# Kernel tuning notes

Measured on AMD Instinct MI355X. Metric: run time of the kernel, lower is better.

The kernel has to match this reference:

```python
import jax, jax.numpy as jnp
import numpy as np

B, N = 8, 512
C_IN, C_E, C_MID, C_OUT = 64, 16, 64, 64


def _linear_params(key, fan_in, fan_out):
    k1, k2 = jax.random.split(key)
    bound = 1.0 / np.sqrt(fan_in)
    W = jax.random.uniform(k1, (fan_out, fan_in), jnp.float32, -bound, bound)
    b = jax.random.uniform(k2, (fan_out,), jnp.float32, -bound, bound)
    return W, b


def setup_inputs() -> dict:
    key = jax.random.key(0)
    ks = jax.random.split(key, 9)
    x = jax.random.normal(ks[0], (B, N, C_IN), jnp.float32)
    adj = jax.random.randint(ks[1], (B, N, N), 0, 2).astype(jnp.float32)
    edge_attr = jax.random.normal(ks[2], (B, N, N, C_E), jnp.float32)
    W1, b1 = _linear_params(ks[3], C_IN, C_MID)
    W2, b2 = _linear_params(ks[4], C_IN, C_MID)
    We, be = _linear_params(ks[5], C_E, C_MID)
    Wn, bn = _linear_params(ks[6], C_MID, C_MID)   # user-supplied net: Linear(mid, mid)
    Wo1, bo1 = _linear_params(ks[7], C_IN, C_OUT)
    Wo2, bo2 = _linear_params(ks[8], C_MID, C_OUT)
    return {"x": x, "adj": adj, "edge_attr": edge_attr,
            "W1": W1, "b1": b1, "W2": W2, "b2": b2, "We": We, "be": be,
            "Wn": Wn, "bn": bn, "Wo1": Wo1, "bo1": bo1, "Wo2": Wo2, "bo2": bo2}


def reference(x, adj, edge_attr, W1, b1, W2, b2, We, be, Wn, bn, Wo1, bo1, Wo2, bo2):
    # node / edge projections
    msg_1 = jnp.einsum('bnc,mc->bnm', x, W1) + b1          # [B, N, mid]
    msg_2 = jnp.einsum('bnc,mc->bnm', x, W2) + b2          # [B, N, mid]
    msg_e = jnp.einsum('bijc,mc->bijm', edge_attr, We) + be  # [B, N, N, mid]
    # broadcast sum: msg_1 over dim 1, msg_2 over dim 2 (matches torch unsqueeze)
    msg = msg_1[:, None, :, :] + msg_2[:, :, None, :] + msg_e  # [B, N, N, mid]
    # net applied after hard-coded relu
    msg = jnp.einsum('bijm,km->bijk', jax.nn.relu(msg), Wn) + bn
    # sum aggregator with adjacency mask, reduced over dim 1
    msg = jnp.einsum('bijm,bij->bjm', msg, adj)            # [B, N, mid]
    h_1 = jnp.einsum('bnc,oc->bno', x, Wo1) + bo1
    h_2 = jnp.einsum('bnm,om->bno', msg, Wo2) + bo2
    return h_1 + h_2
```

## Files before the change

### kernel.cpp

```cpp
#include <hip/hip_runtime.h>
#include <stdint.h>

#define B_   8
#define N_   512
#define CE_  16
#define BN_  (B_*N_)
#define Q_   8

typedef __attribute__((ext_vector_type(8))) short bf16x8;
typedef __attribute__((ext_vector_type(4))) float f32x4;
typedef __attribute__((ext_vector_type(4))) int   i32x4;

union PackA { i32x4 i; bf16x8 h; };

__device__ __forceinline__ unsigned short f2bf_rne(float f) {
  unsigned u = __float_as_uint(f);
  u += 0x7FFFu + ((u >> 16) & 1u);
  return (unsigned short)(u >> 16);
}

__global__ __launch_bounds__(256) void k1_pre(
    const float* __restrict__ x,
    const float* __restrict__ W1,  const float* __restrict__ b1,
    const float* __restrict__ W2,  const float* __restrict__ b2,
    const float* __restrict__ Wn,  const float* __restrict__ bn,
    const float* __restrict__ Wo1, const float* __restrict__ bo1,
    const float* __restrict__ Wo2, const float* __restrict__ bo2,
    float* __restrict__ m1, float* __restrict__ m2t, float* __restrict__ base,
    float* __restrict__ Wc, float* __restrict__ bc)
{
  const int tid = threadIdx.x;
  if (blockIdx.x == BN_/4) {
    for (int idx = tid; idx < 64*64; idx += 256) {
      const int k = idx >> 6, m = idx & 63;
      float acc = 0.f;
      for (int t = 0; t < 64; ++t) acc += Wo2[k*64 + t] * Wn[t*64 + m];
      Wc[idx] = acc;
    }
    if (tid < 64) {
      float acc = 0.f;
      for (int t = 0; t < 64; ++t) acc += Wo2[tid*64 + t] * bn[t];
      bc[tid] = acc;
    }
    return;
  }
  const int r = tid >> 6, m = tid & 63;
  const int row = blockIdx.x*4 + r;
  __shared__ float xs[4][64];
  xs[r][m] = x[(size_t)row*64 + m];
  __syncthreads();
  const float* xr = xs[r];
  float a1 = b1[m], a2 = b2[m], a3 = bo1[m] + bo2[m];
  const float* w1r = W1  + m*64;
  const float* w2r = W2  + m*64;
  const float* w3r = Wo1 + m*64;
  #pragma unroll 8
  for (int c = 0; c < 64; ++c) {
    const float xv = xr[c];
    a1 += xv * w1r[c];
    a2 += xv * w2r[c];
    a3 += xv * w3r[c];
  }
  m1[(size_t)row*64 + m]   = a1;
  m2t[(size_t)row*64 + (m & 15)*4 + (m >> 4)] = a2;
  base[(size_t)row*64 + m] = a3;
}

__global__ __launch_bounds__(256, 5) void k2_main(
    const float* __restrict__ edge, const float* __restrict__ adj,
    const float* __restrict__ We,   const float* __restrict__ be,
    const float* __restrict__ m1,   const float* __restrict__ m2t,
    float* __restrict__ pS, float* __restrict__ pdeg)
{
  const int tid  = threadIdx.x;
  const int lane = tid & 63;
  const int wid  = tid >> 6;
  const int col  = lane & 15;
  const int quad = lane >> 4;

  const int blk = blockIdx.x;
  const int q   = blk & 7;
  const int grp = blk >> 3;
  const int b   = grp >> 5;
  const int j0  = (grp & 31) << 4;
  const int i0  = q*64 + wid*16;

  const i32x4 izero = {0,0,0,0};

  bf16x8 bfr[4];
  #pragma unroll
  for (int c = 0; c < 4; ++c) {
    PackA u; u.i = izero;
    if (quad < 2) {
      const float* wr = We + (c*16 + col)*CE_ + quad*8;
      unsigned p0 = ((unsigned)f2bf_rne(wr[1]) << 16) | f2bf_rne(wr[0]);
      unsigned p1 = ((unsigned)f2bf_rne(wr[3]) << 16) | f2bf_rne(wr[2]);
      unsigned p2 = ((unsigned)f2bf_rne(wr[5]) << 16) | f2bf_rne(wr[4]);
      unsigned p3 = ((unsigned)f2bf_rne(wr[7]) << 16) | f2bf_rne(wr[6]);
      i32x4 v = {(int)p0, (int)p1, (int)p2, (int)p3};
      u.i = v;
    }
    bfr[c] = u.h;
  }

  f32x4 m1f[4];
  #pragma unroll
  for (int c = 0; c < 4; ++c) {
    const float bev = be[c*16 + col];
    const float* mp = m1 + (size_t)(b*N_ + j0 + quad*4)*64 + c*16 + col;
    m1f[c].x = mp[0]   + bev;
    m1f[c].y = mp[64]  + bev;
    m1f[c].z = mp[128] + bev;
    m1f[c].w = mp[192] + bev;
  }

  const f32x4 fzero = {0.f, 0.f, 0.f, 0.f};
  f32x4 S[4];
  S[0] = fzero; S[1] = fzero; S[2] = fzero; S[3] = fzero;
  f32x4 deg4 = fzero;

  const float* ep  = edge + ((size_t)(b*N_ + i0)*N_ + (j0 + col))*CE_ + (quad & 1)*8;
  const float* ap  = adj  + (size_t)(b*N_ + i0)*N_ + j0 + quad*4;
  const float* m2p = m2t  + (size_t)(b*N_ + i0)*64 + col*4;

  f32x4 e0   = *(const f32x4*)(ep);
  f32x4 e1   = *(const f32x4*)(ep + 4);
  f32x4 adj4 = *(const f32x4*)(ap);
  f32x4 m2v  = *(const f32x4*)(m2p);

  auto compute = [&](const f32x4& ce0, const f32x4& ce1,
                     const f32x4& ca, const f32x4& cm) {
    PackA ua;
    ua.i.x = (int)__builtin_amdgcn_perm(__float_as_uint(ce0.y), __float_as_uint(ce0.x), 0x07060302u);
    ua.i.y = (int)__builtin_amdgcn_perm(__float_as_uint(ce0.w), __float_as_uint(ce0.z), 0x07060302u);
    ua.i.z = (int)__builtin_amdgcn_perm(__float_as_uint(ce1.y), __float_as_uint(ce1.x), 0x07060302u);
    ua.i.w = (int)__builtin_amdgcn_perm(__float_as_uint(ce1.w), __float_as_uint(ce1.z), 0x07060302u);
    #pragma unroll
    for (int c = 0; c < 4; ++c) {
      const float m2c = cm[c];
      f32x4 cin;
      cin.x = m1f[c].x + m2c;
      cin.y = m1f[c].y + m2c;
      cin.z = m1f[c].z + m2c;
      cin.w = m1f[c].w + m2c;
      f32x4 r = __builtin_amdgcn_mfma_f32_16x16x32_bf16(ua.h, bfr[c], cin, 0, 0, 0);
      S[c].x += ca.x * fmaxf(r.x, 0.f);
      S[c].y += ca.y * fmaxf(r.y, 0.f);
      S[c].z += ca.z * fmaxf(r.z, 0.f);
      S[c].w += ca.w * fmaxf(r.w, 0.f);
    }
    deg4.x += ca.x; deg4.y += ca.y; deg4.z += ca.z; deg4.w += ca.w;
  };

  #pragma unroll 1
  for (int it = 0; it < 15; ++it) {
    ep  += N_ * CE_;
    ap  += N_;
    m2p += 64;
    const f32x4 ne0  = *(const f32x4*)(ep);
    const f32x4 ne1  = *(const f32x4*)(ep + 4);
    const f32x4 nadj = *(const f32x4*)(ap);
    const f32x4 nm2  = *(const f32x4*)(m2p);
    compute(e0, e1, adj4, m2v);
    e0 = ne0; e1 = ne1; adj4 = nadj; m2v = nm2;
  }
  compute(e0, e1, adj4, m2v);

  __shared__ float red[4][16*68];
  __shared__ float redd[4][16];
  #pragma unroll
  for (int c = 0; c < 4; ++c) {
    red[wid][(quad*4 + 0)*68 + c*16 + col] = S[c].x;
    red[wid][(quad*4 + 1)*68 + c*16 + col] = S[c].y;
    red[wid][(quad*4 + 2)*68 + c*16 + col] = S[c].z;
    red[wid][(quad*4 + 3)*68 + c*16 + col] = S[c].w;
  }
  if (col == 0) {
    redd[wid][quad*4 + 0] = deg4.x;
    redd[wid][quad*4 + 1] = deg4.y;
    redd[wid][quad*4 + 2] = deg4.z;
    redd[wid][quad*4 + 3] = deg4.w;
  }
  __syncthreads();

  float* oS = pS + ((size_t)q*BN_ + b*N_ + j0)*64;
  #pragma unroll
  for (int t = 0; t < 4; ++t) {
    const int idx = t*256 + tid;
    const int row = idx >> 6, ch = idx & 63;
    oS[idx] = red[0][row*68 + ch] + red[1][row*68 + ch]
            + red[2][row*68 + ch] + red[3][row*68 + ch];
  }
  if (tid < 16) {
    pdeg[(size_t)q*BN_ + b*N_ + j0 + tid] =
      redd[0][tid] + redd[1][tid] + redd[2][tid] + redd[3][tid];
  }
}

__global__ __launch_bounds__(256) void k3_out(
    const float* __restrict__ pS, const float* __restrict__ pdeg,
    const float* __restrict__ base, const float* __restrict__ Wc,
    const float* __restrict__ bc, float* __restrict__ out)
{
  const int tid = threadIdx.x;
  const int r   = tid >> 6;
  const int k   = tid & 63;
  const int row = blockIdx.x*4 + r;
  __shared__ float sm[4][64];
  float s = 0.f, dr = 0.f;
  #pragma unroll
  for (int q = 0; q < Q_; ++q) {
    s  += pS[((size_t)q*BN_ + row)*64 + k];
    dr += pdeg[(size_t)q*BN_ + row];
  }
  sm[r][k] = s;
  __syncthreads();
  float acc = base[(size_t)row*64 + k] + dr * bc[k];
  const float* wr  = Wc + k*64;
  const float* smr = sm[r];
  #pragma unroll
  for (int m = 0; m < 64; ++m) acc += smr[m] * wr[m];
  out[(size_t)row*64 + k] = acc;
}

extern "C" void kernel_launch(void* const* d_in, const int* in_sizes, int n_in,
                              void* d_out, int out_size, void* d_ws, size_t ws_size,
                              hipStream_t stream)
{
  const float* x    = (const float*)d_in[0];
  const float* adj  = (const float*)d_in[1];
  const float* edge = (const float*)d_in[2];
  const float* W1   = (const float*)d_in[3];
  const float* b1   = (const float*)d_in[4];
  const float* W2   = (const float*)d_in[5];
  const float* b2   = (const float*)d_in[6];
  const float* We   = (const float*)d_in[7];
  const float* be   = (const float*)d_in[8];
  const float* Wn   = (const float*)d_in[9];
  const float* bn   = (const float*)d_in[10];
  const float* Wo1  = (const float*)d_in[11];
  const float* bo1  = (const float*)d_in[12];
  const float* Wo2  = (const float*)d_in[13];
  const float* bo2  = (const float*)d_in[14];
  float* out = (float*)d_out;

  char* ws = (char*)d_ws;
  float* m1   = (float*)(ws);
  float* m2t  = (float*)(ws + (size_t)(1u<<20));
  float* base = (float*)(ws + (size_t)2*(1u<<20));
  float* Wc   = (float*)(ws + (size_t)3*(1u<<20));
  float* bc   = (float*)(ws + (size_t)3*(1u<<20) + 16384);
  float* pdeg = (float*)(ws + (size_t)3*(1u<<20) + 17408);
  float* pS   = (float*)(ws + (size_t)3*(1u<<20) + 17408 + 131072);

  k1_pre<<<BN_/4 + 1, 256, 0, stream>>>(x, W1, b1, W2, b2, Wn, bn,
                                        Wo1, bo1, Wo2, bo2,
                                        m1, m2t, base, Wc, bc);
  k2_main<<<2048, 256, 0, stream>>>(edge, adj, We, be, m1, m2t, pS, pdeg);
  k3_out<<<BN_/4, 256, 0, stream>>>(pS, pdeg, base, Wc, bc, out);
}
```

Baseline: 302.0 us.

## Fold msg_2 into MFMA via padded K slot and double-buffer the edge loop

The per-row msg_2 term is stored as bf16 and placed into an unused K slot of the MFMA. The A operand gets a constant 1.0 in that slot and the B operand gets the m2 value, so the MFMA adds it directly instead of four vector adds per channel group per iteration. The main loop is also unrolled by two with ping-pong register buffers for the prefetched edge, adj and m2 loads. This cuts VALU work in the inner loop but rounds msg_2 to bf16 and raises register pressure.

Result: slower. 428.2 us (+41.8%).

```diff
diff --git a/kernel.cpp b/kernel.cpp
--- a/kernel.cpp
+++ b/kernel.cpp
@@ -10,6 +10,7 @@
 typedef __attribute__((ext_vector_type(8))) short bf16x8;
 typedef __attribute__((ext_vector_type(4))) float f32x4;
 typedef __attribute__((ext_vector_type(4))) int   i32x4;
+typedef __attribute__((ext_vector_type(2))) unsigned int u32x2;
 
 union PackA { i32x4 i; bf16x8 h; };
 
@@ -26,8 +27,8 @@
     const float* __restrict__ Wn,  const float* __restrict__ bn,
     const float* __restrict__ Wo1, const float* __restrict__ bo1,
     const float* __restrict__ Wo2, const float* __restrict__ bo2,
-    float* __restrict__ m1, float* __restrict__ m2t, float* __restrict__ base,
-    float* __restrict__ Wc, float* __restrict__ bc)
+    float* __restrict__ m1, unsigned short* __restrict__ m2b,
+    float* __restrict__ base, float* __restrict__ Wc, float* __restrict__ bc)
 {
   const int tid = threadIdx.x;
   if (blockIdx.x == BN_/4) {
@@ -62,14 +63,14 @@
     a3 += xv * w3r[c];
   }
   m1[(size_t)row*64 + m]   = a1;
-  m2t[(size_t)row*64 + (m & 15)*4 + (m >> 4)] = a2;
+  m2b[(size_t)row*64 + (m & 15)*4 + (m >> 4)] = f2bf_rne(a2);
   base[(size_t)row*64 + m] = a3;
 }
 
 __global__ __launch_bounds__(256, 5) void k2_main(
     const float* __restrict__ edge, const float* __restrict__ adj,
     const float* __restrict__ We,   const float* __restrict__ be,
-    const float* __restrict__ m1,   const float* __restrict__ m2t,
+    const float* __restrict__ m1,   const unsigned short* __restrict__ m2b,
     float* __restrict__ pS, float* __restrict__ pdeg)
 {
   const int tid  = threadIdx.x;
@@ -87,7 +88,8 @@
 
   const i32x4 izero = {0,0,0,0};
 
-  bf16x8 bfr[4];
+  PackA ub[4];
+  unsigned bx0[4];
   #pragma unroll
   for (int c = 0; c < 4; ++c) {
     PackA u; u.i = izero;
@@ -100,8 +102,13 @@
       i32x4 v = {(int)p0, (int)p1, (int)p2, (int)p3};
       u.i = v;
     }
-    bfr[c] = u.h;
-  }
+    ub[c] = u;
+    bx0[c] = (unsigned)u.i.x;
+  }
+
+  const unsigned sel   = (quad == 2) ? 0xFFFFu : 0u;
+  const unsigned akeep = (quad == 2) ? 0xFFFF0000u : 0xFFFFFFFFu;
+  const unsigned ains  = (quad == 2) ? 0x00003F80u : 0u;
 
   f32x4 m1f[4];
   #pragma unroll
@@ -119,31 +126,27 @@
   S[0] = fzero; S[1] = fzero; S[2] = fzero; S[3] = fzero;
   f32x4 deg4 = fzero;
 
-  const float* ep  = edge + ((size_t)(b*N_ + i0)*N_ + (j0 + col))*CE_ + (quad & 1)*8;
-  const float* ap  = adj  + (size_t)(b*N_ + i0)*N_ + j0 + quad*4;
-  const float* m2p = m2t  + (size_t)(b*N_ + i0)*64 + col*4;
-
-  f32x4 e0   = *(const f32x4*)(ep);
-  f32x4 e1   = *(const f32x4*)(ep + 4);
-  f32x4 adj4 = *(const f32x4*)(ap);
-  f32x4 m2v  = *(const f32x4*)(m2p);
+  const float*          ep = edge + ((size_t)(b*N_ + i0)*N_ + (j0 + col))*CE_ + (quad & 1)*8;
+  const float*          ap = adj  + (size_t)(b*N_ + i0)*N_ + j0 + quad*4;
+  const unsigned short* mp = m2b  + (size_t)(b*N_ + i0)*64 + col*4;
 
   auto compute = [&](const f32x4& ce0, const f32x4& ce1,
-                     const f32x4& ca, const f32x4& cm) {
+                     const f32x4& ca, const u32x2& cm) {
     PackA ua;
-    ua.i.x = (int)__builtin_amdgcn_perm(__float_as_uint(ce0.y), __float_as_uint(ce0.x), 0x07060302u);
+    unsigned ax = (unsigned)__builtin_amdgcn_perm(__float_as_uint(ce0.y), __float_as_uint(ce0.x), 0x07060302u);
+    ua.i.x = (int)((ax & akeep) | ains);
     ua.i.y = (int)__builtin_amdgcn_perm(__float_as_uint(ce0.w), __float_as_uint(ce0.z), 0x07060302u);
     ua.i.z = (int)__builtin_amdgcn_perm(__float_as_uint(ce1.y), __float_as_uint(ce1.x), 0x07060302u);
     ua.i.w = (int)__builtin_amdgcn_perm(__float_as_uint(ce1.w), __float_as_uint(ce1.z), 0x07060302u);
+    const unsigned mc0 = cm.x & 0xFFFFu, mc1 = cm.x >> 16;
+    const unsigned mc2 = cm.y & 0xFFFFu, mc3 = cm.y >> 16;
+    ub[0].i.x = (int)(bx0[0] | (mc0 & sel));
+    ub[1].i.x = (int)(bx0[1] | (mc1 & sel));
+    ub[2].i.x = (int)(bx0[2] | (mc2 & sel));
+    ub[3].i.x = (int)(bx0[3] | (mc3 & sel));
     #pragma unroll
     for (int c = 0; c < 4; ++c) {
-      const float m2c = cm[c];
-      f32x4 cin;
-      cin.x = m1f[c].x + m2c;
-      cin.y = m1f[c].y + m2c;
-      cin.z = m1f[c].z + m2c;
-      cin.w = m1f[c].w + m2c;
-      f32x4 r = __builtin_amdgcn_mfma_f32_16x16x32_bf16(ua.h, bfr[c], cin, 0, 0, 0);
+      f32x4 r = __builtin_amdgcn_mfma_f32_16x16x32_bf16(ua.h, ub[c].h, m1f[c], 0, 0, 0);
       S[c].x += ca.x * fmaxf(r.x, 0.f);
       S[c].y += ca.y * fmaxf(r.y, 0.f);
       S[c].z += ca.z * fmaxf(r.z, 0.f);
@@ -152,19 +155,28 @@
     deg4.x += ca.x; deg4.y += ca.y; deg4.z += ca.z; deg4.w += ca.w;
   };
 
+  f32x4 e0a = *(const f32x4*)(ep);
+  f32x4 e1a = *(const f32x4*)(ep + 4);
+  f32x4 ada = *(const f32x4*)(ap);
+  u32x2 ma  = *(const u32x2*)(mp);
+  f32x4 e0b, e1b, adb; u32x2 mb;
+
   #pragma unroll 1
-  for (int it = 0; it < 15; ++it) {
-    ep  += N_ * CE_;
-    ap  += N_;
-    m2p += 64;
-    const f32x4 ne0  = *(const f32x4*)(ep);
-    const f32x4 ne1  = *(const f32x4*)(ep + 4);
-    const f32x4 nadj = *(const f32x4*)(ap);
-    const f32x4 nm2  = *(const f32x4*)(m2p);
-    compute(e0, e1, adj4, m2v);
-    e0 = ne0; e1 = ne1; adj4 = nadj; m2v = nm2;
-  }
-  compute(e0, e1, adj4, m2v);
+  for (int it = 0; it < 16; it += 2) {
+    ep += N_ * CE_; ap += N_; mp += 64;
+    e0b = *(const f32x4*)(ep);
+    e1b = *(const f32x4*)(ep + 4);
+    adb = *(const f32x4*)(ap);
+    mb  = *(const u32x2*)(mp);
+    compute(e0a, e1a, ada, ma);
+    const int adv = (it < 14) ? 1 : 0;
+    ep += adv * (N_ * CE_); ap += adv * N_; mp += adv * 64;
+    e0a = *(const f32x4*)(ep);
+    e1a = *(const f32x4*)(ep + 4);
+    ada = *(const f32x4*)(ap);
+    ma  = *(const u32x2*)(mp);
+    compute(e0b, e1b, adb, mb);
+  }
 
   __shared__ float red[4][16*68];
   __shared__ float redd[4][16];
@@ -245,17 +257,17 @@
   float* out = (float*)d_out;
 
   char* ws = (char*)d_ws;
-  float* m1   = (float*)(ws);
-  float* m2t  = (float*)(ws + (size_t)(1u<<20));
-  float* base = (float*)(ws + (size_t)2*(1u<<20));
-  float* Wc   = (float*)(ws + (size_t)3*(1u<<20));
-  float* bc   = (float*)(ws + (size_t)3*(1u<<20) + 16384);
-  float* pdeg = (float*)(ws + (size_t)3*(1u<<20) + 17408);
-  float* pS   = (float*)(ws + (size_t)3*(1u<<20) + 17408 + 131072);
+  float*          m1   = (float*)(ws);
+  unsigned short* m2b  = (unsigned short*)(ws + (size_t)(1u<<20));
+  float*          base = (float*)(ws + (size_t)2*(1u<<20));
+  float*          Wc   = (float*)(ws + (size_t)3*(1u<<20));
+  float*          bc   = (float*)(ws + (size_t)3*(1u<<20) + 16384);
+  float*          pdeg = (float*)(ws + (size_t)3*(1u<<20) + 17408);
+  float*          pS   = (float*)(ws + (size_t)3*(1u<<20) + 17408 + 131072);
 
   k1_pre<<<BN_/4 + 1, 256, 0, stream>>>(x, W1, b1, W2, b2, Wn, bn,
                                         Wo1, bo1, Wo2, bo2,
-                                        m1, m2t, base, Wc, bc);
-  k2_main<<<2048, 256, 0, stream>>>(edge, adj, We, be, m1, m2t, pS, pdeg);
+                                        m1, m2b, base, Wc, bc);
+  k2_main<<<2048, 256, 0, stream>>>(edge, adj, We, be, m1, m2b, pS, pdeg);
   k3_out<<<BN_/4, 256, 0, stream>>>(pS, pdeg, base, Wc, bc, out);
 }
```

## Prefetch edge tiles into LDS with a 4-slot async global_load_lds ring

Applied to the files above, without the earlier changes.

Edge-attribute loads in the main aggregation kernel now go through a per-wave 4-slot LDS ring filled by global_load_lds, replacing the single-step register double buffer. Adjacency and m2 values sit in a matching 4-deep register ring, so three iterations of loads are in flight while one is computed. This targets the load latency the kernel is bound by. The ring uses more LDS and registers, so the launch bound drops from 5 to 4 blocks per SM, which lowers occupancy. The reduction scratch reuses the same LDS buffer, and correctness depends on a hand-written vmcnt wait plus in-order completion of loads.

Measured after the change: 448.9 us. 1.49x slower.

```diff
diff --git a/kernel.cpp b/kernel.cpp
--- a/kernel.cpp
+++ b/kernel.cpp
@@ -12,6 +12,9 @@
 typedef __attribute__((ext_vector_type(4))) int   i32x4;
 
 union PackA { i32x4 i; bf16x8 h; };
+
+typedef const __attribute__((address_space(1))) void cg_void;
+typedef __attribute__((address_space(3))) void ls_void;
 
 __device__ __forceinline__ unsigned short f2bf_rne(float f) {
   unsigned u = __float_as_uint(f);
@@ -66,12 +69,15 @@
   base[(size_t)row*64 + m] = a3;
 }
 
-__global__ __launch_bounds__(256, 5) void k2_main(
+__global__ __launch_bounds__(256, 4) void k2_main(
     const float* __restrict__ edge, const float* __restrict__ adj,
     const float* __restrict__ We,   const float* __restrict__ be,
     const float* __restrict__ m1,   const float* __restrict__ m2t,
     float* __restrict__ pS, float* __restrict__ pdeg)
 {
+  __shared__ f32x4 smem4[4][512];
+  __shared__ float redd[4][16];
+
   const int tid  = threadIdx.x;
   const int lane = tid & 63;
   const int wid  = tid >> 6;
@@ -107,11 +113,11 @@
   #pragma unroll
   for (int c = 0; c < 4; ++c) {
     const float bev = be[c*16 + col];
-    const float* mp = m1 + (size_t)(b*N_ + j0 + quad*4)*64 + c*16 + col;
-    m1f[c].x = mp[0]   + bev;
-    m1f[c].y = mp[64]  + bev;
-    m1f[c].z = mp[128] + bev;
-    m1f[c].w = mp[192] + bev;
+    const float* mp1 = m1 + (size_t)(b*N_ + j0 + quad*4)*64 + c*16 + col;
+    m1f[c].x = mp1[0]   + bev;
+    m1f[c].y = mp1[64]  + bev;
+    m1f[c].z = mp1[128] + bev;
+    m1f[c].w = mp1[192] + bev;
   }
 
   const f32x4 fzero = {0.f, 0.f, 0.f, 0.f};
@@ -119,14 +125,19 @@
   S[0] = fzero; S[1] = fzero; S[2] = fzero; S[3] = fzero;
   f32x4 deg4 = fzero;
 
-  const float* ep  = edge + ((size_t)(b*N_ + i0)*N_ + (j0 + col))*CE_ + (quad & 1)*8;
-  const float* ap  = adj  + (size_t)(b*N_ + i0)*N_ + j0 + quad*4;
-  const float* m2p = m2t  + (size_t)(b*N_ + i0)*64 + col*4;
-
-  f32x4 e0   = *(const f32x4*)(ep);
-  f32x4 e1   = *(const f32x4*)(ep + 4);
-  f32x4 adj4 = *(const f32x4*)(ap);
-  f32x4 m2v  = *(const f32x4*)(m2p);
+  const float* ep = edge + ((size_t)(b*N_ + i0)*N_ + (j0 + col))*CE_ + (quad & 1)*8;
+  const float* ap = adj  + (size_t)(b*N_ + i0)*N_ + j0 + quad*4;
+  const float* mp = m2t  + (size_t)(b*N_ + i0)*64 + col*4;
+  const int STEP = N_ * CE_;
+
+  f32x4* sbase = &smem4[wid][0];
+
+  auto issue_edge = [&](int slot, const float* p) {
+    __builtin_amdgcn_global_load_lds((cg_void*)p,
+        (ls_void*)(sbase + slot*128), 16, 0, 0);
+    __builtin_amdgcn_global_load_lds((cg_void*)(p + 4),
+        (ls_void*)(sbase + slot*128 + 64), 16, 0, 0);
+  };
 
   auto compute = [&](const f32x4& ce0, const f32x4& ce1,
                      const f32x4& ca, const f32x4& cm) {
@@ -152,28 +163,43 @@
     deg4.x += ca.x; deg4.y += ca.y; deg4.z += ca.z; deg4.w += ca.w;
   };
 
+  f32x4 adjR[4], m2R[4];
+  #pragma unroll
+  for (int g = 0; g < 3; ++g) {
+    issue_edge(g, ep);
+    adjR[g] = *(const f32x4*)ap;
+    m2R[g]  = *(const f32x4*)mp;
+    ep += STEP; ap += N_; mp += 64;
+  }
+  int itI = 3;
+
   #pragma unroll 1
-  for (int it = 0; it < 15; ++it) {
-    ep  += N_ * CE_;
-    ap  += N_;
-    m2p += 64;
-    const f32x4 ne0  = *(const f32x4*)(ep);
-    const f32x4 ne1  = *(const f32x4*)(ep + 4);
-    const f32x4 nadj = *(const f32x4*)(ap);
-    const f32x4 nm2  = *(const f32x4*)(m2p);
-    compute(e0, e1, adj4, m2v);
-    e0 = ne0; e1 = ne1; adj4 = nadj; m2v = nm2;
-  }
-  compute(e0, e1, adj4, m2v);
-
-  __shared__ float red[4][16*68];
-  __shared__ float redd[4][16];
+  for (int o = 0; o < 4; ++o) {
+    #pragma unroll
+    for (int kk = 0; kk < 4; ++kk) {
+      if (itI < 16) {
+        const int slot = (kk + 3) & 3;
+        issue_edge(slot, ep);
+        adjR[slot] = *(const f32x4*)ap;
+        m2R[slot]  = *(const f32x4*)mp;
+        ep += STEP; ap += N_; mp += 64;
+        ++itI;
+      }
+      __builtin_amdgcn_s_waitcnt(0x0F7C);
+      const f32x4 e0 = sbase[kk*128 + lane];
+      const f32x4 e1 = sbase[kk*128 + 64 + lane];
+      compute(e0, e1, adjR[kk], m2R[kk]);
+    }
+  }
+
+  float* redf  = (float*)&smem4[0][0];
+  float* myred = redf + wid*2048;
   #pragma unroll
   for (int c = 0; c < 4; ++c) {
-    red[wid][(quad*4 + 0)*68 + c*16 + col] = S[c].x;
-    red[wid][(quad*4 + 1)*68 + c*16 + col] = S[c].y;
-    red[wid][(quad*4 + 2)*68 + c*16 + col] = S[c].z;
-    red[wid][(quad*4 + 3)*68 + c*16 + col] = S[c].w;
+    myred[(quad*4 + 0)*68 + c*16 + col] = S[c].x;
+    myred[(quad*4 + 1)*68 + c*16 + col] = S[c].y;
+    myred[(quad*4 + 2)*68 + c*16 + col] = S[c].z;
+    myred[(quad*4 + 3)*68 + c*16 + col] = S[c].w;
   }
   if (col == 0) {
     redd[wid][quad*4 + 0] = deg4.x;
@@ -188,8 +214,8 @@
   for (int t = 0; t < 4; ++t) {
     const int idx = t*256 + tid;
     const int row = idx >> 6, ch = idx & 63;
-    oS[idx] = red[0][row*68 + ch] + red[1][row*68 + ch]
-            + red[2][row*68 + ch] + red[3][row*68 + ch];
+    oS[idx] = redf[0*2048 + row*68 + ch] + redf[1*2048 + row*68 + ch]
+            + redf[2*2048 + row*68 + ch] + redf[3*2048 + row*68 + ch];
   }
   if (tid < 16) {
     pdeg[(size_t)q*BN_ + b*N_ + j0 + tid] =
```

## Skip edge_attr loads for zero-adjacency entries and double-buffer the main loop

Applied to the files above, without the earlier changes.

Each lane now reads its own adjacency scalar ahead of time. For masked-out (i,j) pairs, and for the quads whose B fragment is zero, it points the edge_attr vector load at a small cached dummy address (the We weights) instead of the real row. This cuts HBM traffic on the dominant edge tensor, since garbage values there are multiplied by a zero adjacency or a zero weight fragment. The loop is also unrolled by two with explicit A/B register buffers and a two-step lookahead on the adjacency scalars. The cost is a data-dependent address that adds latency, plus sector-granularity limits on how much traffic is actually saved.

Result: slower. 368.4 us (+22.0%).

```diff
diff --git a/kernel.cpp b/kernel.cpp
--- a/kernel.cpp
+++ b/kernel.cpp
@@ -86,12 +86,14 @@
   const int i0  = q*64 + wid*16;
 
   const i32x4 izero = {0,0,0,0};
+  const bool  q01   = (quad < 2);
+  const float* dummy = We;
 
   bf16x8 bfr[4];
   #pragma unroll
   for (int c = 0; c < 4; ++c) {
     PackA u; u.i = izero;
-    if (quad < 2) {
+    if (q01) {
       const float* wr = We + (c*16 + col)*CE_ + quad*8;
       unsigned p0 = ((unsigned)f2bf_rne(wr[1]) << 16) | f2bf_rne(wr[0]);
       unsigned p1 = ((unsigned)f2bf_rne(wr[3]) << 16) | f2bf_rne(wr[2]);
@@ -107,11 +109,11 @@
   #pragma unroll
   for (int c = 0; c < 4; ++c) {
     const float bev = be[c*16 + col];
-    const float* mp = m1 + (size_t)(b*N_ + j0 + quad*4)*64 + c*16 + col;
-    m1f[c].x = mp[0]   + bev;
-    m1f[c].y = mp[64]  + bev;
-    m1f[c].z = mp[128] + bev;
-    m1f[c].w = mp[192] + bev;
+    const float* mp1 = m1 + (size_t)(b*N_ + j0 + quad*4)*64 + c*16 + col;
+    m1f[c].x = mp1[0]   + bev;
+    m1f[c].y = mp1[64]  + bev;
+    m1f[c].z = mp1[128] + bev;
+    m1f[c].w = mp1[192] + bev;
   }
 
   const f32x4 fzero = {0.f, 0.f, 0.f, 0.f};
@@ -121,12 +123,22 @@
 
   const float* ep  = edge + ((size_t)(b*N_ + i0)*N_ + (j0 + col))*CE_ + (quad & 1)*8;
   const float* ap  = adj  + (size_t)(b*N_ + i0)*N_ + j0 + quad*4;
-  const float* m2p = m2t  + (size_t)(b*N_ + i0)*64 + col*4;
-
-  f32x4 e0   = *(const f32x4*)(ep);
-  f32x4 e1   = *(const f32x4*)(ep + 4);
-  f32x4 adj4 = *(const f32x4*)(ap);
-  f32x4 m2v  = *(const f32x4*)(m2p);
+  const float* mp  = m2t  + (size_t)(b*N_ + i0)*64 + col*4;
+  const float* apc0 = adj + (size_t)(b*N_ + i0)*N_ + j0 + col;
+  const float* apc  = apc0;
+  const int STEP = N_ * CE_;
+
+  const float ac0 = apc[0];
+  float ac1 = apc[N_];
+  float ac2 = apc[2*N_];
+  apc += 3*N_;
+
+  const float* pe = (q01 && ac0 != 0.f) ? ep : dummy;
+  f32x4 e0a  = *(const f32x4*)(pe);
+  f32x4 e1a  = *(const f32x4*)(pe + 4);
+  f32x4 ada  = *(const f32x4*)(ap);
+  f32x4 ma4  = *(const f32x4*)(mp);
+  f32x4 e0b, e1b, adb, mb4;
 
   auto compute = [&](const f32x4& ce0, const f32x4& ce1,
                      const f32x4& ca, const f32x4& cm) {
@@ -153,18 +165,28 @@
   };
 
   #pragma unroll 1
-  for (int it = 0; it < 15; ++it) {
-    ep  += N_ * CE_;
-    ap  += N_;
-    m2p += 64;
-    const f32x4 ne0  = *(const f32x4*)(ep);
-    const f32x4 ne1  = *(const f32x4*)(ep + 4);
-    const f32x4 nadj = *(const f32x4*)(ap);
-    const f32x4 nm2  = *(const f32x4*)(m2p);
-    compute(e0, e1, adj4, m2v);
-    e0 = ne0; e1 = ne1; adj4 = nadj; m2v = nm2;
-  }
-  compute(e0, e1, adj4, m2v);
+  for (int it = 0; it < 16; it += 2) {
+    ep += STEP; ap += N_; mp += 64;
+    pe  = (q01 && ac1 != 0.f) ? ep : dummy;
+    e0b = *(const f32x4*)(pe);
+    e1b = *(const f32x4*)(pe + 4);
+    adb = *(const f32x4*)(ap);
+    mb4 = *(const f32x4*)(mp);
+    const float acn0 = *((it + 3 < 16) ? apc : apc0);
+    apc += N_;
+    compute(e0a, e1a, ada, ma4);
+    const int adv = (it < 14) ? 1 : 0;
+    ep += adv * STEP; ap += adv * N_; mp += adv * 64;
+    pe  = (q01 && ac2 != 0.f) ? ep : dummy;
+    e0a = *(const f32x4*)(pe);
+    e1a = *(const f32x4*)(pe + 4);
+    ada = *(const f32x4*)(ap);
+    ma4 = *(const f32x4*)(mp);
+    const float acn1 = *((it + 4 < 16) ? apc : apc0);
+    apc += N_;
+    compute(e0b, e1b, adb, mb4);
+    ac1 = acn0; ac2 = acn1;
+  }
 
   __shared__ float red[4][16*68];
   __shared__ float redd[4][16];
```
